# Kernel tuning notes

Hardware: AMD Instinct MI355X
Metric: run time of the kernel (lower is better)

The kernel has to match this reference:

```python
import jax, jax.numpy as jnp
import numpy as np

PARA_CH = 256
FEATURE_CH = 256
PI = 3.14159  # matches the literal in the torch source


def _linear_params(key, fan_in, fan_out):
    kw, kb = jax.random.split(key)
    bound = 1.0 / np.sqrt(fan_in)
    W = jax.random.uniform(kw, (fan_in, fan_out), minval=-bound, maxval=bound, dtype=jnp.float32)
    b = jax.random.uniform(kb, (fan_out,), minval=-bound, maxval=bound, dtype=jnp.float32)
    return W, b


def setup_inputs() -> dict:
    key = jax.random.key(0)
    ks = jax.random.split(key, 6)
    feature_map = jax.random.normal(ks[0], (4, FEATURE_CH, 128, 128), dtype=jnp.float32)
    para_code = jax.random.normal(ks[1], (4, PARA_CH), dtype=jnp.float32)
    W1, b1 = _linear_params(ks[2], PARA_CH, PARA_CH)
    Ws, bs = _linear_params(ks[3], PARA_CH, FEATURE_CH)
    Wr, br = _linear_params(ks[4], PARA_CH, FEATURE_CH)
    Wt, bt = _linear_params(ks[5], PARA_CH, 2 * FEATURE_CH)
    return {"feature_map": feature_map, "para_code": para_code,
            "W1": W1, "b1": b1, "Ws": Ws, "bs": bs,
            "Wr": Wr, "br": br, "Wt": Wt, "bt": bt}


def _coord_1d(n):
    # align_corners=True-style normalized coordinates, as in make_coordinate_grid_3d
    return 2.0 * (jnp.arange(n, dtype=jnp.float32) / (n - 1)) - 1.0


def _trilinear_sample_zeros(vol, gx, gy, gz):
    """F.grid_sample 5D equivalent: mode='bilinear' (trilinear), padding_mode='zeros',
    align_corners=False. vol: [B,D,H,W] (channel dim of size 1 squeezed out);
    gx,gy,gz: [B,Do,Ho,Wo] normalized coords. Returns [B,Do,Ho,Wo]."""
    B, D, H, W = vol.shape
    ix = ((gx + 1.0) * W - 1.0) * 0.5
    iy = ((gy + 1.0) * H - 1.0) * 0.5
    iz = ((gz + 1.0) * D - 1.0) * 0.5
    x0f, y0f, z0f = jnp.floor(ix), jnp.floor(iy), jnp.floor(iz)
    wx, wy, wz = ix - x0f, iy - y0f, iz - z0f
    x0 = x0f.astype(jnp.int32); x1 = x0 + 1
    y0 = y0f.astype(jnp.int32); y1 = y0 + 1
    z0 = z0f.astype(jnp.int32); z1 = z0 + 1
    vflat = vol.reshape(B, -1)

    def gather(zi, yi, xi):
        valid = (zi >= 0) & (zi < D) & (yi >= 0) & (yi < H) & (xi >= 0) & (xi < W)
        zc = jnp.clip(zi, 0, D - 1)
        yc = jnp.clip(yi, 0, H - 1)
        xc = jnp.clip(xi, 0, W - 1)
        flat = (zc * H + yc) * W + xc  # [B,Do,Ho,Wo]
        v = jnp.take_along_axis(vflat, flat.reshape(B, -1), axis=1).reshape(flat.shape)
        return jnp.where(valid, v, 0.0)

    out = (gather(z0, y0, x0) * (1 - wz) * (1 - wy) * (1 - wx)
           + gather(z0, y0, x1) * (1 - wz) * (1 - wy) * wx
           + gather(z0, y1, x0) * (1 - wz) * wy * (1 - wx)
           + gather(z0, y1, x1) * (1 - wz) * wy * wx
           + gather(z1, y0, x0) * wz * (1 - wy) * (1 - wx)
           + gather(z1, y0, x1) * wz * (1 - wy) * wx
           + gather(z1, y1, x0) * wz * wy * (1 - wx)
           + gather(z1, y1, x1) * wz * wy * wx)
    return out


def reference(feature_map, para_code, W1, b1, Ws, bs, Wr, br, Wt, bt):
    B, C, H, W = feature_map.shape  # C == feature_ch == depth of 3D grid
    p = jax.nn.relu(para_code @ W1 + b1)                      # [B, para_ch]
    scale = jax.nn.sigmoid(p @ Ws + bs) * 2.0                 # [B, C]
    angle = jnp.tanh(p @ Wr + br) * PI                        # [B, C]
    translation = jnp.tanh(p @ Wt + bt).reshape(B, C, 2)      # [B, C, 2]
    ca, sa = jnp.cos(angle), jnp.sin(angle)
    # rotation matrix [[cos, -sin], [sin, cos]] per (batch, channel)
    rot = jnp.stack([jnp.stack([ca, -sa], -1), jnp.stack([sa, ca], -1)], -2)  # [B,C,2,2]

    x = _coord_1d(W)  # [W]
    y = _coord_1d(H)  # [H]
    z = _coord_1d(C)  # [C] (depth == channel dim)
    grid_xy = jnp.stack(jnp.broadcast_arrays(x[None, None, :], y[None, :, None]), -1)  # [1,H,W,2] -> broadcast to [C,H,W,2]
    grid_xy = jnp.broadcast_to(grid_xy, (C, H, W, 2))

    # per-pixel affine transform: rot @ [x,y] * scale + trans
    trans_grid = jnp.einsum('bcij,chwj->bchwi', rot, grid_xy)
    trans_grid = trans_grid * scale[:, :, None, None, None] + translation[:, :, None, None, :]
    gx = trans_grid[..., 0]
    gy = trans_grid[..., 1]
    gz = jnp.broadcast_to(z[None, :, None, None], (B, C, H, W))

    return _trilinear_sample_zeros(feature_map, gx, gy, gz)  # [B,C,H,W]
```

## Files before the change

### kernel.cpp

```cpp
#include <hip/hip_runtime.h>
#include <math.h>

#define BATCH 4
#define CH    256
#define HH    128
#define WW    128
#define PC    256
#define PI_F  3.14159f
#define PLANE (HH * WW)
#define NP    4

#define PSTRIDE 134
#define PROWS   131
#define BUFSZ   (PROWS * PSTRIDE)

__device__ __forceinline__ void barrier_lds() {
    asm volatile("s_waitcnt lgkmcnt(0)\n\ts_barrier" ::: "memory");
}

struct Stage { float4 a[4]; float4 b[4]; };

__device__ __forceinline__ Stage stage_load(const float* __restrict__ pl0,
                                            const float* __restrict__ pl1, int t) {
    Stage s;
#pragma unroll
    for (int j = 0; j < 4; ++j) {
        const int f = 4 * (t + 1024 * j);
        s.a[j] = *(const float4*)(pl0 + f);
        s.b[j] = *(const float4*)(pl1 + f);
    }
    return s;
}

__device__ __forceinline__ void stage_store_pad(float* __restrict__ buf, const Stage& s,
                                                float wz0, float wz1, int t) {
#pragma unroll
    for (int j = 0; j < 4; ++j) {
        const int f = 4 * (t + 1024 * j);
        const int y = f >> 7, x = f & (WW - 1);
        float* p = &buf[(y + 1) * PSTRIDE + (x + 1)];
        p[0] = fmaf(wz0, s.a[j].x, wz1 * s.b[j].x);
        p[1] = fmaf(wz0, s.a[j].y, wz1 * s.b[j].y);
        p[2] = fmaf(wz0, s.a[j].z, wz1 * s.b[j].z);
        p[3] = fmaf(wz0, s.a[j].w, wz1 * s.b[j].w);
    }
}

__device__ __forceinline__ void gather_plane(const float* __restrict__ buf,
                                             const float4 P,
                                             float* __restrict__ outp,
                                             const float yf, const int xi) {
    const float cA  = P.x, cB = P.y;
    float ixp = fmaf(cA, (float)xi, fmaf(-cB, yf, P.z));
    float iyp = fmaf(cB, (float)xi, fmaf( cA, yf, P.w));
    const float dx8 = 8.0f * cA, dy8 = 8.0f * cB;
#pragma unroll 4
    for (int k = 0; k < 16; ++k) {
        const float xc  = fminf(fmaxf(ixp, 0.0f), 129.99f);
        const float yc  = fminf(fmaxf(iyp, 0.0f), 129.99f);
        const float x0f = floorf(xc), y0f = floorf(yc);
        const float fx  = xc - x0f,   fy  = yc - y0f;
        const int   a   = (int)y0f * PSTRIDE + (int)x0f;
        const float v00 = buf[a],           v01 = buf[a + 1];
        const float v10 = buf[a + PSTRIDE], v11 = buf[a + PSTRIDE + 1];
        const float h0  = fmaf(fx, v01 - v00, v00);
        const float h1  = fmaf(fx, v11 - v10, v10);
        outp[k * 8 + xi] = fmaf(fy, h1 - h0, h0);
        ixp += dx8; iyp += dy8;
    }
}

__global__ __launch_bounds__(1024, 4)
void adaat_fused_kernel(const float* __restrict__ fm,
                        const float* __restrict__ pc,
                        const float* __restrict__ W1, const float* __restrict__ b1,
                        const float* __restrict__ Ws, const float* __restrict__ bs,
                        const float* __restrict__ Wr, const float* __restrict__ br,
                        const float* __restrict__ Wt, const float* __restrict__ bt,
                        float* __restrict__ out) {
    __shared__ float  lds[2 * BUFSZ];
    __shared__ float  red[1024];
    __shared__ float  p_sh[PC];
    __shared__ float  sh_head[16];
    __shared__ float4 sh_par[NP];

    const int t   = threadIdx.x;
    const int bc0 = blockIdx.x * NP;
    const int b   = bc0 >> 8;

    const float* base = fm + (size_t)b * (CH * PLANE);
    const float* pl0[NP]; const float* pl1[NP];
    float w0[NP], w1[NP];
#pragma unroll
    for (int i = 0; i < NP; ++i) {
        const int   c  = (bc0 + i) & (CH - 1);
        const float iz = (256.0f / 255.0f) * (float)c - 0.5f;
        const float zf = floorf(iz);
        const float fz = iz - zf;
        const int   z0 = (int)zf;
        w0[i]  = (z0 >= 0)     ? (1.0f - fz) : 0.0f;
        w1[i]  = (z0 + 1 < CH) ? fz          : 0.0f;
        pl0[i] = base + (size_t)max(z0, 0)          * PLANE;
        pl1[i] = base + (size_t)min(z0 + 1, CH - 1) * PLANE;
    }

    Stage s = stage_load(pl0[0], pl1[0], t);

#pragma unroll
    for (int i = 0; i < 35; ++i) {
        const int idx = t + 1024 * i;
        if (idx < 2 * BUFSZ) lds[idx] = 0.0f;
    }

    {
        const int jj = t & 255, kk = t >> 8;
        const float* pcb = pc + b * PC + kk * 64;
        const float* w   = W1 + (kk * 64) * PC + jj;
        float acc = 0.0f;
#pragma unroll 8
        for (int i = 0; i < 64; ++i)
            acc = fmaf(pcb[i], w[i * PC], acc);
        red[t] = acc;
    }
    barrier_lds();
    if (t < 256)
        p_sh[t] = fmaxf(red[t] + red[256 + t] + red[512 + t] + red[768 + t] + b1[t], 0.0f);
    barrier_lds();

    stage_store_pad(&lds[0], s, w0[0], w1[0], t);

    const int wv = t >> 6, l = t & 63;
    {
        const int q  = wv >> 2;
        const int h  = wv & 3;
        const int cq = (bc0 + q) & (CH - 1);
        const float* wp; int stride;
        if      (h == 0) { wp = Ws + cq;                stride = PC;     }
        else if (h == 1) { wp = Wr + cq;                stride = PC;     }
        else             { wp = Wt + 2 * cq + (h == 3); stride = 2 * PC; }
        float dot = 0.0f;
#pragma unroll
        for (int m = 0; m < 4; ++m) {
            const int k = l + 64 * m;
            dot = fmaf(p_sh[k], wp[(size_t)k * stride], dot);
        }
#pragma unroll
        for (int off = 32; off >= 1; off >>= 1)
            dot += __shfl_xor(dot, off, 64);
        if (l == 0) sh_head[wv] = dot;
    }
    barrier_lds();

    if (t < NP) {
        const int cq = (bc0 + t) & (CH - 1);
        const float s2  = 2.0f / (1.0f + expf(-(sh_head[4 * t] + bs[cq])));
        const float ang = tanhf(sh_head[4 * t + 1] + br[cq]) * PI_F;
        float sa, ca;
        sincosf(ang, &sa, &ca);
        const float A  = s2 * ca, B = s2 * sa;
        const float Tx = tanhf(sh_head[4 * t + 2] + bt[2 * cq]);
        const float Ty = tanhf(sh_head[4 * t + 3] + bt[2 * cq + 1]);
        sh_par[t] = make_float4(A * (128.0f / 127.0f),
                                B * (128.0f / 127.0f),
                                64.0f * (Tx - A + B) + 64.5f,
                                64.0f * (Ty - A - B) + 64.5f);
    }
    barrier_lds();

    const int   xi = l & 7;
    const int   yj = wv * 8 + (l >> 3);
    const float yf = (float)yj;

#pragma unroll
    for (int i = 1; i < NP; ++i) {
        s = stage_load(pl0[i], pl1[i], t);
        gather_plane(&lds[((i - 1) & 1) * BUFSZ], sh_par[i - 1],
                     out + (size_t)(bc0 + i - 1) * PLANE + yj * WW, yf, xi);
        stage_store_pad(&lds[(i & 1) * BUFSZ], s, w0[i], w1[i], t);
        barrier_lds();
    }
    gather_plane(&lds[((NP - 1) & 1) * BUFSZ], sh_par[NP - 1],
                 out + (size_t)(bc0 + NP - 1) * PLANE + yj * WW, yf, xi);
}

extern "C" void kernel_launch(void* const* d_in, const int* in_sizes, int n_in,
                              void* d_out, int out_size, void* d_ws, size_t ws_size,
                              hipStream_t stream) {
    const float* feature_map = (const float*)d_in[0];
    const float* para_code   = (const float*)d_in[1];
    const float* W1 = (const float*)d_in[2];
    const float* b1 = (const float*)d_in[3];
    const float* Ws = (const float*)d_in[4];
    const float* bs = (const float*)d_in[5];
    const float* Wr = (const float*)d_in[6];
    const float* br = (const float*)d_in[7];
    const float* Wt = (const float*)d_in[8];
    const float* bt = (const float*)d_in[9];

    adaat_fused_kernel<<<BATCH * CH / NP, 1024, 0, stream>>>(
        feature_map, para_code, W1, b1, Ws, bs, Wr, br, Wt, bt, (float*)d_out);
}
```

Measured before the change: 151.5 us.

## Process one channel plane per block with swizzled block order and row-contiguous gather

Each block now handles a single (batch, channel) plane instead of four, which removes the double-buffered LDS pipeline and halves the shared-memory footprint. The launch bounds are raised so more blocks can be resident per CU. Blocks are remapped with a swizzle so that concurrently running blocks touch different channels. The gather now writes whole contiguous 64-wide rows per wave for coalesced stores. The cost is that the W1 matvec prologue is recomputed four times as often, and the overlap between loading the next plane and gathering the current one is lost.

```diff
diff --git a/kernel.cpp b/kernel.cpp
--- a/kernel.cpp
+++ b/kernel.cpp
@@ -8,7 +8,6 @@
 #define PC    256
 #define PI_F  3.14159f
 #define PLANE (HH * WW)
-#define NP    4
 
 #define PSTRIDE 134
 #define PROWS   131
@@ -46,31 +45,7 @@
     }
 }
 
-__device__ __forceinline__ void gather_plane(const float* __restrict__ buf,
-                                             const float4 P,
-                                             float* __restrict__ outp,
-                                             const float yf, const int xi) {
-    const float cA  = P.x, cB = P.y;
-    float ixp = fmaf(cA, (float)xi, fmaf(-cB, yf, P.z));
-    float iyp = fmaf(cB, (float)xi, fmaf( cA, yf, P.w));
-    const float dx8 = 8.0f * cA, dy8 = 8.0f * cB;
-#pragma unroll 4
-    for (int k = 0; k < 16; ++k) {
-        const float xc  = fminf(fmaxf(ixp, 0.0f), 129.99f);
-        const float yc  = fminf(fmaxf(iyp, 0.0f), 129.99f);
-        const float x0f = floorf(xc), y0f = floorf(yc);
-        const float fx  = xc - x0f,   fy  = yc - y0f;
-        const int   a   = (int)y0f * PSTRIDE + (int)x0f;
-        const float v00 = buf[a],           v01 = buf[a + 1];
-        const float v10 = buf[a + PSTRIDE], v11 = buf[a + PSTRIDE + 1];
-        const float h0  = fmaf(fx, v01 - v00, v00);
-        const float h1  = fmaf(fx, v11 - v10, v10);
-        outp[k * 8 + xi] = fmaf(fy, h1 - h0, h0);
-        ixp += dx8; iyp += dy8;
-    }
-}
-
-__global__ __launch_bounds__(1024, 4)
+__global__ __launch_bounds__(1024, 8)
 void adaat_fused_kernel(const float* __restrict__ fm,
                         const float* __restrict__ pc,
                         const float* __restrict__ W1, const float* __restrict__ b1,
@@ -78,38 +53,35 @@
                         const float* __restrict__ Wr, const float* __restrict__ br,
                         const float* __restrict__ Wt, const float* __restrict__ bt,
                         float* __restrict__ out) {
-    __shared__ float  lds[2 * BUFSZ];
+    __shared__ float  lds[BUFSZ];
     __shared__ float  red[1024];
     __shared__ float  p_sh[PC];
-    __shared__ float  sh_head[16];
-    __shared__ float4 sh_par[NP];
+    __shared__ float  sh_head[4];
+    __shared__ float4 sh_par;
 
-    const int t   = threadIdx.x;
-    const int bc0 = blockIdx.x * NP;
-    const int b   = bc0 >> 8;
+    const int t = threadIdx.x;
+
+    const int bid = blockIdx.x;
+    const int lc  = ((bid & 7) << 7) | (bid >> 3);
+    const int b   = lc >> 8;
+    const int c   = lc & (CH - 1);
 
     const float* base = fm + (size_t)b * (CH * PLANE);
-    const float* pl0[NP]; const float* pl1[NP];
-    float w0[NP], w1[NP];
-#pragma unroll
-    for (int i = 0; i < NP; ++i) {
-        const int   c  = (bc0 + i) & (CH - 1);
-        const float iz = (256.0f / 255.0f) * (float)c - 0.5f;
-        const float zf = floorf(iz);
-        const float fz = iz - zf;
-        const int   z0 = (int)zf;
-        w0[i]  = (z0 >= 0)     ? (1.0f - fz) : 0.0f;
-        w1[i]  = (z0 + 1 < CH) ? fz          : 0.0f;
-        pl0[i] = base + (size_t)max(z0, 0)          * PLANE;
-        pl1[i] = base + (size_t)min(z0 + 1, CH - 1) * PLANE;
-    }
+    const float  iz = (256.0f / 255.0f) * (float)c - 0.5f;
+    const float  zf = floorf(iz);
+    const float  fz = iz - zf;
+    const int    z0 = (int)zf;
+    const float  w0 = (z0 >= 0)     ? (1.0f - fz) : 0.0f;
+    const float  w1 = (z0 + 1 < CH) ? fz          : 0.0f;
+    const float* pl0 = base + (size_t)max(z0, 0)          * PLANE;
+    const float* pl1 = base + (size_t)min(z0 + 1, CH - 1) * PLANE;
 
-    Stage s = stage_load(pl0[0], pl1[0], t);
+    Stage s = stage_load(pl0, pl1, t);
 
 #pragma unroll
-    for (int i = 0; i < 35; ++i) {
+    for (int i = 0; i < 18; ++i) {
         const int idx = t + 1024 * i;
-        if (idx < 2 * BUFSZ) lds[idx] = 0.0f;
+        if (idx < BUFSZ) lds[idx] = 0.0f;
     }
 
     {
@@ -127,17 +99,14 @@
         p_sh[t] = fmaxf(red[t] + red[256 + t] + red[512 + t] + red[768 + t] + b1[t], 0.0f);
     barrier_lds();
 
-    stage_store_pad(&lds[0], s, w0[0], w1[0], t);
+    stage_store_pad(lds, s, w0, w1, t);
 
     const int wv = t >> 6, l = t & 63;
-    {
-        const int q  = wv >> 2;
-        const int h  = wv & 3;
-        const int cq = (bc0 + q) & (CH - 1);
+    if (wv < 4) {
         const float* wp; int stride;
-        if      (h == 0) { wp = Ws + cq;                stride = PC;     }
-        else if (h == 1) { wp = Wr + cq;                stride = PC;     }
-        else             { wp = Wt + 2 * cq + (h == 3); stride = 2 * PC; }
+        if      (wv == 0) { wp = Ws + c;               stride = PC;     }
+        else if (wv == 1) { wp = Wr + c;               stride = PC;     }
+        else              { wp = Wt + 2 * c + (wv == 3); stride = 2 * PC; }
         float dot = 0.0f;
 #pragma unroll
         for (int m = 0; m < 4; ++m) {
@@ -151,36 +120,51 @@
     }
     barrier_lds();
 
-    if (t < NP) {
-        const int cq = (bc0 + t) & (CH - 1);
-        const float s2  = 2.0f / (1.0f + expf(-(sh_head[4 * t] + bs[cq])));
-        const float ang = tanhf(sh_head[4 * t + 1] + br[cq]) * PI_F;
+    if (t == 0) {
+        const float s2  = 2.0f / (1.0f + expf(-(sh_head[0] + bs[c])));
+        const float ang = tanhf(sh_head[1] + br[c]) * PI_F;
         float sa, ca;
         sincosf(ang, &sa, &ca);
         const float A  = s2 * ca, B = s2 * sa;
-        const float Tx = tanhf(sh_head[4 * t + 2] + bt[2 * cq]);
-        const float Ty = tanhf(sh_head[4 * t + 3] + bt[2 * cq + 1]);
-        sh_par[t] = make_float4(A * (128.0f / 127.0f),
-                                B * (128.0f / 127.0f),
-                                64.0f * (Tx - A + B) + 64.5f,
-                                64.0f * (Ty - A - B) + 64.5f);
+        const float Tx = tanhf(sh_head[2] + bt[2 * c]);
+        const float Ty = tanhf(sh_head[3] + bt[2 * c + 1]);
+        sh_par = make_float4(A * (128.0f / 127.0f),
+                             B * (128.0f / 127.0f),
+                             64.0f * (Tx - A + B) + 64.5f,
+                             64.0f * (Ty - A - B) + 64.5f);
     }
     barrier_lds();
 
-    const int   xi = l & 7;
-    const int   yj = wv * 8 + (l >> 3);
-    const float yf = (float)yj;
-
+    {
+        const float4 P  = sh_par;
+        const float  cA = P.x, cB = P.y;
+        float* outp = out + (size_t)lc * PLANE;
+        const float xf0 = (float)l;
+        float rowf = (float)(wv * 8);
+#pragma unroll 2
+        for (int r = 0; r < 8; ++r) {
+            const float bx = fmaf(-cB, rowf, P.z);
+            const float by = fmaf( cA, rowf, P.w);
+            float* orow = outp + (wv * 8 + r) * WW;
 #pragma unroll
-    for (int i = 1; i < NP; ++i) {
-        s = stage_load(pl0[i], pl1[i], t);
-        gather_plane(&lds[((i - 1) & 1) * BUFSZ], sh_par[i - 1],
-                     out + (size_t)(bc0 + i - 1) * PLANE + yj * WW, yf, xi);
-        stage_store_pad(&lds[(i & 1) * BUFSZ], s, w0[i], w1[i], t);
-        barrier_lds();
+            for (int h = 0; h < 2; ++h) {
+                const float xf  = xf0 + 64.0f * h;
+                const float ix  = fmaf(cA, xf, bx);
+                const float iy  = fmaf(cB, xf, by);
+                const float xc  = fminf(fmaxf(ix, 0.0f), 129.99f);
+                const float yc  = fminf(fmaxf(iy, 0.0f), 129.99f);
+                const float x0f = floorf(xc), y0f = floorf(yc);
+                const float fx  = xc - x0f,   fy  = yc - y0f;
+                const int   a   = (int)y0f * PSTRIDE + (int)x0f;
+                const float v00 = lds[a],           v01 = lds[a + 1];
+                const float v10 = lds[a + PSTRIDE], v11 = lds[a + PSTRIDE + 1];
+                const float h0  = fmaf(fx, v01 - v00, v00);
+                const float h1  = fmaf(fx, v11 - v10, v10);
+                orow[h * 64 + l] = fmaf(fy, h1 - h0, h0);
+            }
+            rowf += 1.0f;
+        }
     }
-    gather_plane(&lds[((NP - 1) & 1) * BUFSZ], sh_par[NP - 1],
-                 out + (size_t)(bc0 + NP - 1) * PLANE + yj * WW, yf, xi);
 }
 
 extern "C" void kernel_launch(void* const* d_in, const int* in_sizes, int n_in,
@@ -197,6 +181,6 @@
     const float* Wt = (const float*)d_in[8];
     const float* bt = (const float*)d_in[9];
 
-    adaat_fused_kernel<<<BATCH * CH / NP, 1024, 0, stream>>>(
+    adaat_fused_kernel<<<BATCH * CH, 1024, 0, stream>>>(
         feature_map, para_code, W1, b1, Ws, bs, Wr, br, Wt, bt, (float*)d_out);
 }
```

New measurement: 156.8 us. 1.03x slower.
